# Optimization experiments

Measured on AMD Instinct MI355X. Metric: run time of the kernel, lower is better.

The kernel has to match this reference:

```python
import jax, jax.numpy as jnp
import numpy as np

EMB = 1024
HEADS = 16
HEAD_DIM = EMB // HEADS
SCALE = HEAD_DIM ** -0.5


def setup_inputs() -> dict:
    key = jax.random.key(0)
    ks = jax.random.split(key, 6)
    b, n = 4, 2048
    x = jax.random.normal(ks[0], (b, n, EMB), dtype=jnp.float32)
    ln_w = jnp.ones((EMB,), jnp.float32)
    ln_b = jnp.zeros((EMB,), jnp.float32)
    w_qkv = jax.random.normal(ks[1], (EMB, 3 * EMB), jnp.float32) * (EMB ** -0.5)
    b_qkv = jax.random.normal(ks[2], (3 * EMB,), jnp.float32) * 0.02
    w_proj = jax.random.normal(ks[3], (EMB, EMB), jnp.float32) * (EMB ** -0.5)
    b_proj = jax.random.normal(ks[4], (EMB,), jnp.float32) * 0.02
    return {"x": x, "ln_w": ln_w, "ln_b": ln_b, "w_qkv": w_qkv,
            "b_qkv": b_qkv, "w_proj": w_proj, "b_proj": b_proj}


def reference(x, ln_w, ln_b, w_qkv, b_qkv, w_proj, b_proj):
    res = x
    # LayerNorm over last dim
    mu = jnp.mean(x, axis=-1, keepdims=True)
    var = jnp.var(x, axis=-1, keepdims=True)
    h = (x - mu) * jax.lax.rsqrt(var + 1e-5) * ln_w + ln_b
    b, n, _ = h.shape
    # qkv: last dim split as (heads, head_dim, 3) -- qkv interleaved fastest
    y = h @ w_qkv + b_qkv                      # [b, n, 3E]
    y = y.reshape(b, n, HEADS, HEAD_DIM, 3)
    q, k, v = y[..., 0], y[..., 1], y[..., 2]  # [b, n, h, d]
    scores = jnp.einsum('bqhd,bkhd->bhqk', q, k) * SCALE
    att = jax.nn.softmax(scores, axis=-1)      # dropout p=0 -> identity
    out = jnp.einsum('bhqk,bkhd->bqhd', att, v)
    out = out.reshape(b, n, EMB)
    out = out @ w_proj + b_proj
    return out + res
```

## Files before the change

### kernel.cpp

```cpp
#include <hip/hip_runtime.h>
#include <math.h>

#define EMB 1024
#define HEADS 16
#define HDIM 64
#define NBATCH 4
#define SEQ 2048
#define ROWS (NBATCH * SEQ)
#define SCALE 0.125f
#define QPRESCALE 0.18033688011112042f

typedef float f32x4 __attribute__((ext_vector_type(4)));
typedef float f32x16 __attribute__((ext_vector_type(16)));
typedef short bf16x8 __attribute__((ext_vector_type(8)));

__device__ inline unsigned short f2bf(float f) {
    unsigned int u = __builtin_bit_cast(unsigned int, f);
    u += 0x7fffu + ((u >> 16) & 1u);
    return (unsigned short)(u >> 16);
}
__device__ inline float exp2fast(float x) {
    float y;
    asm("v_exp_f32 %0, %1" : "=v"(y) : "v"(x));
    return y;
}
__device__ inline unsigned int packbf(float x, float y) {
    return __builtin_amdgcn_perm(__builtin_bit_cast(unsigned int, y),
                                 __builtin_bit_cast(unsigned int, x), 0x07060302u);
}
__device__ inline bf16x8 mkfrag(unsigned int a, unsigned int b,
                                unsigned int c, unsigned int d) {
    union { unsigned int u[4]; bf16x8 v; } t;
    t.u[0] = a; t.u[1] = b; t.u[2] = c; t.u[3] = d;
    return t.v;
}

__global__ __launch_bounds__(256) void ln_kernel(const float* __restrict__ x,
                                                 const float* __restrict__ w,
                                                 const float* __restrict__ b,
                                                 unsigned short* __restrict__ h) {
    int row = blockIdx.x;
    const float* xr = x + (size_t)row * EMB;
    unsigned short* hr = h + (size_t)row * EMB;
    float4 v = ((const float4*)xr)[threadIdx.x];
    float s  = v.x + v.y + v.z + v.w;
    float ss = v.x*v.x + v.y*v.y + v.z*v.z + v.w*v.w;
    #pragma unroll
    for (int o = 32; o; o >>= 1) { s += __shfl_xor(s, o); ss += __shfl_xor(ss, o); }
    __shared__ float red[8];
    int wid = threadIdx.x >> 6;
    if ((threadIdx.x & 63) == 0) { red[wid] = s; red[4 + wid] = ss; }
    __syncthreads();
    if (threadIdx.x == 0) {
        red[0] = red[0] + red[1] + red[2] + red[3];
        red[4] = red[4] + red[5] + red[6] + red[7];
    }
    __syncthreads();
    float mu  = red[0] * (1.f / EMB);
    float var = red[4] * (1.f / EMB) - mu * mu;
    float rstd = rsqrtf(var + 1e-5f);
    float4 wv = ((const float4*)w)[threadIdx.x];
    float4 bv = ((const float4*)b)[threadIdx.x];
    ushort4 o;
    o.x = f2bf((v.x - mu) * rstd * wv.x + bv.x);
    o.y = f2bf((v.y - mu) * rstd * wv.y + bv.y);
    o.z = f2bf((v.z - mu) * rstd * wv.z + bv.z);
    o.w = f2bf((v.w - mu) * rstd * wv.w + bv.w);
    ((ushort4*)hr)[threadIdx.x] = o;
}

__global__ __launch_bounds__(256) void wconv(const float* __restrict__ W,
                                             unsigned short* __restrict__ WT,
                                             int N, int perm) {
    __shared__ float t[32][33];
    int k0 = blockIdx.x * 32, n0 = blockIdx.y * 32;
    int tx = threadIdx.x & 31, ty = threadIdx.x >> 5;
    #pragma unroll
    for (int i = 0; i < 32; i += 8)
        t[ty + i][tx] = W[(size_t)(k0 + ty + i) * N + n0 + tx];
    __syncthreads();
    #pragma unroll
    for (int i = 0; i < 32; i += 8) {
        int n = n0 + ty + i;
        int dst = n;
        if (perm) {
            int head = n / 192;
            int rem = n - head * 192;
            int d = rem / 3;
            int which = rem - d * 3;
            dst = which * 1024 + head * 64 + d;
        }
        WT[(size_t)dst * EMB + k0 + tx] = f2bf(t[tx][ty + i]);
    }
}

#define GSTAGE(LDSBUF, GPTR) do {                                                              \
    _Pragma("unroll")                                                                          \
    for (int i_ = 0; i_ < 2; ++i_) {                                                           \
        int slot_ = i_ * 256 + tid;                                                            \
        int row_ = slot_ >> 2, c8_ = (slot_ & 3) * 8;                                          \
        __builtin_amdgcn_global_load_lds(                                                      \
            (const __attribute__((address_space(1))) void*)((GPTR) + (size_t)row_ * EMB + c8_),\
            (__attribute__((address_space(3))) void*)((char*)(LDSBUF) + i_ * 4096 + w * 1024), \
            16, 0, 0);                                                                         \
    }                                                                                          \
} while (0)

__global__ __launch_bounds__(256) void qkv_mfma(const unsigned short* __restrict__ A,
                                                const unsigned short* __restrict__ BT,
                                                const float* __restrict__ bias,
                                                unsigned short* __restrict__ qo,
                                                unsigned short* __restrict__ ko,
                                                unsigned short* __restrict__ vo) {
    __shared__ alignas(16) unsigned short As[128][32];
    __shared__ alignas(16) unsigned short Bs[128][32];
    int tid = threadIdx.x;
    int w = tid >> 6, lane = tid & 63, lg = lane >> 4, lr = lane & 15;
    int wr = w >> 1, wc = w & 1;
    int bid = blockIdx.x;
    int local = bid >> 3;
    int bm = (bid & 7) * 8 + (local & 7);
    int bn = local >> 3;
    const unsigned short* Ab = A + (size_t)(bm * 128) * EMB;
    const unsigned short* Bb = BT + (size_t)(bn * 128) * EMB;
    f32x4 acc[4][4];
    #pragma unroll
    for (int m = 0; m < 4; ++m)
        #pragma unroll
        for (int n = 0; n < 4; ++n) acc[m][n] = (f32x4){0.f, 0.f, 0.f, 0.f};
    for (int k0 = 0; k0 < EMB; k0 += 32) {
        GSTAGE(As, Ab + k0);
        GSTAGE(Bs, Bb + k0);
        __syncthreads();
        bf16x8 af[4], bf[4];
        #pragma unroll
        for (int m = 0; m < 4; ++m) af[m] = *(const bf16x8*)&As[wr * 64 + m * 16 + lr][lg * 8];
        #pragma unroll
        for (int n = 0; n < 4; ++n) bf[n] = *(const bf16x8*)&Bs[wc * 64 + n * 16 + lr][lg * 8];
        #pragma unroll
        for (int m = 0; m < 4; ++m)
            #pragma unroll
            for (int n = 0; n < 4; ++n)
                acc[m][n] = __builtin_amdgcn_mfma_f32_16x16x32_bf16(af[m], bf[n], acc[m][n], 0, 0, 0);
        __syncthreads();
    }
    #pragma unroll
    for (int n = 0; n < 4; ++n) {
        int cp = bn * 128 + wc * 64 + n * 16 + lr;
        int which = cp >> 10;
        int head = (cp >> 6) & 15;
        int d = cp & 63;
        float bv = bias[head * 192 + d * 3 + which];
        #pragma unroll
        for (int m = 0; m < 4; ++m) {
            #pragma unroll
            for (int r = 0; r < 4; ++r) {
                int row = bm * 128 + wr * 64 + m * 16 + lg * 4 + r;
                int bb = row >> 11;
                int nq = row & 2047;
                float val = acc[m][n][r] + bv;
                if (which == 0)
                    qo[(((size_t)bb * HEADS + head) * SEQ + nq) * HDIM + d] = f2bf(val * QPRESCALE);
                else if (which == 1)
                    ko[(((size_t)bb * HEADS + head) * SEQ + nq) * HDIM + d] = f2bf(val);
                else
                    vo[(((size_t)bb * HEADS + head) * HDIM + d) * SEQ + nq] = f2bf(val);
            }
        }
    }
}

#define STAGE(nb, kb_) do {                                                                        \
    int off_ = sbase + lane * 16;                                   \
    int row_ = off_ >> 7;                                                                          \
    int lg_  = off_ ^ ((row_ & 7) << 4);                            \
    __builtin_amdgcn_global_load_lds(                                                              \
        (const __attribute__((address_space(1))) void*)(kbytes + (size_t)(kb_) * 8192 + lg_),      \
        (__attribute__((address_space(3))) void*)(&kls[nb][sbase]), 16, 0, 0);                     \
    __builtin_amdgcn_global_load_lds(                                                              \
        (const __attribute__((address_space(1))) void*)(vbytes + (size_t)row_ * (SEQ * 2)          \
                                         + (size_t)(kb_) * 128 + (lg_ & 127)),                     \
        (__attribute__((address_space(3))) void*)(&vls[nb][sbase]), 16, 0, 0);                     \
} while (0)

__global__ __launch_bounds__(512) void attn_mfma(const unsigned short* __restrict__ Q,
                                                 const unsigned short* __restrict__ K,
                                                 const unsigned short* __restrict__ VT,
                                                 unsigned short* __restrict__ AO) {
    __shared__ alignas(16) unsigned char kls[2][8192];
    __shared__ alignas(16) unsigned char vls[2][8192];
    int tid = threadIdx.x;
    int w = tid >> 6, lane = tid & 63;
    int col = lane & 31;
    int hi  = lane >> 5;
    int bid = blockIdx.x;
    int swz = (bid & 7) * 64 + (bid >> 3);
    int b  = swz >> 7;
    int hh = (swz >> 3) & 15;
    int qt = swz & 7;
    int q0 = qt * 256 + w * 32;
    size_t bh = ((size_t)b * HEADS + hh) * (size_t)SEQ * HDIM;
    const unsigned short* qp = Q + bh + (size_t)(q0 + col) * HDIM + 8 * hi;
    bf16x8 qB0 = *(const bf16x8*)(qp);
    bf16x8 qB1 = *(const bf16x8*)(qp + 16);
    bf16x8 qB2 = *(const bf16x8*)(qp + 32);
    bf16x8 qB3 = *(const bf16x8*)(qp + 48);
    f32x16 o0 = {0.f,0.f,0.f,0.f,0.f,0.f,0.f,0.f,0.f,0.f,0.f,0.f,0.f,0.f,0.f,0.f};
    f32x16 o1 = {0.f,0.f,0.f,0.f,0.f,0.f,0.f,0.f,0.f,0.f,0.f,0.f,0.f,0.f,0.f,0.f};
    float l = 0.f;
    const char* kbytes = (const char*)(K + bh);
    const char* vbytes = (const char*)(VT + bh);
    const int NT = SEQ / 64;
    int sbase = w * 1024;

    STAGE(0, 0);
    __syncthreads();
    for (int kb = 0; kb < NT; ++kb) {
        int cur = kb & 1;
        if (kb + 1 < NT) STAGE(cur ^ 1, kb + 1);
        const char* kcur = (const char*)&kls[cur][0];
        const char* vcur = (const char*)&vls[cur][0];
        #pragma unroll
        for (int t = 0; t < 2; ++t) {
            int keyl = t * 32 + col;
            int ksw = (keyl & 7) << 4;
            int kbs = keyl * 128;
            bf16x8 kf0 = *(const bf16x8*)(kcur + ((kbs +  0 + hi * 16) ^ ksw));
            bf16x8 kf1 = *(const bf16x8*)(kcur + ((kbs + 32 + hi * 16) ^ ksw));
            bf16x8 kf2 = *(const bf16x8*)(kcur + ((kbs + 64 + hi * 16) ^ ksw));
            bf16x8 kf3 = *(const bf16x8*)(kcur + ((kbs + 96 + hi * 16) ^ ksw));
            f32x16 s = {0.f,0.f,0.f,0.f,0.f,0.f,0.f,0.f,0.f,0.f,0.f,0.f,0.f,0.f,0.f,0.f};
            __builtin_amdgcn_s_setprio(1);
            s = __builtin_amdgcn_mfma_f32_32x32x16_bf16(kf0, qB0, s, 0, 0, 0);
            s = __builtin_amdgcn_mfma_f32_32x32x16_bf16(kf1, qB1, s, 0, 0, 0);
            s = __builtin_amdgcn_mfma_f32_32x32x16_bf16(kf2, qB2, s, 0, 0, 0);
            s = __builtin_amdgcn_mfma_f32_32x32x16_bf16(kf3, qB3, s, 0, 0, 0);
            __builtin_amdgcn_s_setprio(0);
            float p[16];
            float lsa = 0.f, lsb = 0.f;
            #pragma unroll
            for (int r = 0; r < 16; r += 2) {
                p[r]     = exp2fast(s[r]);
                p[r + 1] = exp2fast(s[r + 1]);
                lsa += p[r];
                lsb += p[r + 1];
            }
            l += lsa + lsb;
            unsigned int pk0 = packbf(p[0], p[1]),   pk1 = packbf(p[2], p[3]);
            unsigned int pk2 = packbf(p[4], p[5]),   pk3 = packbf(p[6], p[7]);
            unsigned int pk4 = packbf(p[8], p[9]),   pk5 = packbf(p[10], p[11]);
            unsigned int pk6 = packbf(p[12], p[13]), pk7 = packbf(p[14], p[15]);
            asm volatile("v_permlane32_swap_b32 %0, %1" : "+v"(pk0), "+v"(pk2));
            asm volatile("v_permlane32_swap_b32 %0, %1" : "+v"(pk1), "+v"(pk3));
            asm volatile("v_permlane32_swap_b32 %0, %1" : "+v"(pk4), "+v"(pk6));
            asm volatile("v_permlane32_swap_b32 %0, %1" : "+v"(pk5), "+v"(pk7));
            bf16x8 pf0 = mkfrag(pk0, pk1, pk2, pk3);
            bf16x8 pf1 = mkfrag(pk4, pk5, pk6, pk7);
            int vsw = (col & 7) << 4;
            int vb0 = col * 128 + t * 64;
            int vb1 = (32 + col) * 128 + t * 64;
            bf16x8 vf00 = *(const bf16x8*)(vcur + ((vb0 + hi * 16) ^ vsw));
            bf16x8 vf01 = *(const bf16x8*)(vcur + ((vb0 + 32 + hi * 16) ^ vsw));
            bf16x8 vf10 = *(const bf16x8*)(vcur + ((vb1 + hi * 16) ^ vsw));
            bf16x8 vf11 = *(const bf16x8*)(vcur + ((vb1 + 32 + hi * 16) ^ vsw));
            __builtin_amdgcn_s_setprio(1);
            o0 = __builtin_amdgcn_mfma_f32_32x32x16_bf16(pf0, vf00, o0, 0, 0, 0);
            o0 = __builtin_amdgcn_mfma_f32_32x32x16_bf16(pf1, vf01, o0, 0, 0, 0);
            o1 = __builtin_amdgcn_mfma_f32_32x32x16_bf16(pf0, vf10, o1, 0, 0, 0);
            o1 = __builtin_amdgcn_mfma_f32_32x32x16_bf16(pf1, vf11, o1, 0, 0, 0);
            __builtin_amdgcn_s_setprio(0);
        }
        if (kb + 1 < NT) __syncthreads();
    }
    float invc = 1.f / (l + __shfl_xor(l, 32));
    #pragma unroll
    for (int reg = 0; reg < 16; ++reg) {
        int crow = (reg & 3) + 8 * (reg >> 2) + 4 * hi;
        float invr = __shfl(invc, crow);
        int qq = q0 + crow;
        unsigned short* op = AO + ((size_t)b * SEQ + qq) * EMB + hh * HDIM + col;
        op[0]  = f2bf(o0[reg] * invr);
        op[32] = f2bf(o1[reg] * invr);
    }
}

__global__ __launch_bounds__(256) void proj_mfma(const unsigned short* __restrict__ A,
                                                 const unsigned short* __restrict__ BT,
                                                 const float* __restrict__ bias,
                                                 const float* __restrict__ resid,
                                                 float* __restrict__ out) {
    __shared__ alignas(16) unsigned short As[128][32];
    __shared__ alignas(16) unsigned short Bs[128][32];
    int tid = threadIdx.x;
    int w = tid >> 6, lane = tid & 63, lg = lane >> 4, lr = lane & 15;
    int wr = w >> 1, wc = w & 1;
    int bid = blockIdx.x;
    int local = bid >> 3;
    int bm = (bid & 7) * 8 + (local & 7);
    int bn = local >> 3;
    const unsigned short* Ab = A + (size_t)(bm * 128) * EMB;
    const unsigned short* Bb = BT + (size_t)(bn * 128) * EMB;
    f32x4 acc[4][4];
    #pragma unroll
    for (int m = 0; m < 4; ++m)
        #pragma unroll
        for (int n = 0; n < 4; ++n) acc[m][n] = (f32x4){0.f, 0.f, 0.f, 0.f};
    for (int k0 = 0; k0 < EMB; k0 += 32) {
        GSTAGE(As, Ab + k0);
        GSTAGE(Bs, Bb + k0);
        __syncthreads();
        bf16x8 af[4], bf[4];
        #pragma unroll
        for (int m = 0; m < 4; ++m) af[m] = *(const bf16x8*)&As[wr * 64 + m * 16 + lr][lg * 8];
        #pragma unroll
        for (int n = 0; n < 4; ++n) bf[n] = *(const bf16x8*)&Bs[wc * 64 + n * 16 + lr][lg * 8];
        #pragma unroll
        for (int m = 0; m < 4; ++m)
            #pragma unroll
            for (int n = 0; n < 4; ++n)
                acc[m][n] = __builtin_amdgcn_mfma_f32_16x16x32_bf16(af[m], bf[n], acc[m][n], 0, 0, 0);
        __syncthreads();
    }
    #pragma unroll
    for (int n = 0; n < 4; ++n) {
        int c = bn * 128 + wc * 64 + n * 16 + lr;
        float bv = bias[c];
        #pragma unroll
        for (int m = 0; m < 4; ++m) {
            #pragma unroll
            for (int r = 0; r < 4; ++r) {
                size_t row = (size_t)bm * 128 + wr * 64 + m * 16 + lg * 4 + r;
                out[row * EMB + c] = acc[m][n][r] + bv + resid[row * EMB + c];
            }
        }
    }
}

extern "C" void kernel_launch(void* const* d_in, const int* in_sizes, int n_in,
                              void* d_out, int out_size, void* d_ws, size_t ws_size,
                              hipStream_t stream) {
    const float* x      = (const float*)d_in[0];
    const float* ln_w   = (const float*)d_in[1];
    const float* ln_b   = (const float*)d_in[2];
    const float* w_qkv  = (const float*)d_in[3];
    const float* b_qkv  = (const float*)d_in[4];
    const float* w_proj = (const float*)d_in[5];
    const float* b_proj = (const float*)d_in[6];
    float* out = (float*)d_out;

    char* ws = (char*)d_ws;
    const size_t MB16 = (size_t)ROWS * EMB * sizeof(unsigned short);
    unsigned short* h   = (unsigned short*)ws;
    unsigned short* q   = (unsigned short*)(ws + MB16);
    unsigned short* k   = (unsigned short*)(ws + 2 * MB16);
    unsigned short* v   = (unsigned short*)(ws + 3 * MB16);
    unsigned short* ao  = (unsigned short*)(ws + 4 * MB16);
    unsigned short* wqT = (unsigned short*)(ws + 5 * MB16);
    unsigned short* wpT = (unsigned short*)(ws + 5 * MB16 + (size_t)3 * EMB * EMB * 2);

    wconv<<<dim3(EMB / 32, 3 * EMB / 32), 256, 0, stream>>>(w_qkv, wqT, 3 * EMB, 1);
    wconv<<<dim3(EMB / 32, EMB / 32), 256, 0, stream>>>(w_proj, wpT, EMB, 0);
    ln_kernel<<<ROWS, 256, 0, stream>>>(x, ln_w, ln_b, h);
    qkv_mfma<<<1536, 256, 0, stream>>>(h, wqT, b_qkv, q, k, v);
    attn_mfma<<<512, 512, 0, stream>>>(q, k, v, ao);
    proj_mfma<<<512, 256, 0, stream>>>(ao, wpT, b_proj, x, out);
}
```

Baseline: 219.8 us.

## Double-buffer LDS tiles in QKV and projection GEMMs to overlap loads with MFMA

Both GEMM kernels now use two LDS buffers per operand and issue the global-to-LDS loads for the next K tile before computing on the current one. This drops one barrier per iteration and is meant to hide global load latency behind MFMA work. The cost is doubled LDS use per block, which can lower occupancy. There is also a risk of ordering hazards, because the async global_load_lds writes are only ordered by the single remaining barrier.

After: 230.9 us. 1.05x slower.

```diff
diff --git a/kernel.cpp b/kernel.cpp
--- a/kernel.cpp
+++ b/kernel.cpp
@@ -112,8 +112,8 @@
                                                 unsigned short* __restrict__ qo,
                                                 unsigned short* __restrict__ ko,
                                                 unsigned short* __restrict__ vo) {
-    __shared__ alignas(16) unsigned short As[128][32];
-    __shared__ alignas(16) unsigned short Bs[128][32];
+    __shared__ alignas(16) unsigned short As[2][128][32];
+    __shared__ alignas(16) unsigned short Bs[2][128][32];
     int tid = threadIdx.x;
     int w = tid >> 6, lane = tid & 63, lg = lane >> 4, lr = lane & 15;
     int wr = w >> 1, wc = w & 1;
@@ -128,21 +128,27 @@
     for (int m = 0; m < 4; ++m)
         #pragma unroll
         for (int n = 0; n < 4; ++n) acc[m][n] = (f32x4){0.f, 0.f, 0.f, 0.f};
-    for (int k0 = 0; k0 < EMB; k0 += 32) {
-        GSTAGE(As, Ab + k0);
-        GSTAGE(Bs, Bb + k0);
-        __syncthreads();
+    const int NI = EMB / 32;
+    GSTAGE(As[0], Ab);
+    GSTAGE(Bs[0], Bb);
+    __syncthreads();
+    for (int it = 0; it < NI; ++it) {
+        int cur = it & 1;
+        if (it + 1 < NI) {
+            GSTAGE(As[cur ^ 1], Ab + (it + 1) * 32);
+            GSTAGE(Bs[cur ^ 1], Bb + (it + 1) * 32);
+        }
         bf16x8 af[4], bf[4];
         #pragma unroll
-        for (int m = 0; m < 4; ++m) af[m] = *(const bf16x8*)&As[wr * 64 + m * 16 + lr][lg * 8];
-        #pragma unroll
-        for (int n = 0; n < 4; ++n) bf[n] = *(const bf16x8*)&Bs[wc * 64 + n * 16 + lr][lg * 8];
+        for (int m = 0; m < 4; ++m) af[m] = *(const bf16x8*)&As[cur][wr * 64 + m * 16 + lr][lg * 8];
+        #pragma unroll
+        for (int n = 0; n < 4; ++n) bf[n] = *(const bf16x8*)&Bs[cur][wc * 64 + n * 16 + lr][lg * 8];
         #pragma unroll
         for (int m = 0; m < 4; ++m)
             #pragma unroll
             for (int n = 0; n < 4; ++n)
                 acc[m][n] = __builtin_amdgcn_mfma_f32_16x16x32_bf16(af[m], bf[n], acc[m][n], 0, 0, 0);
-        __syncthreads();
+        if (it + 1 < NI) __syncthreads();
     }
     #pragma unroll
     for (int n = 0; n < 4; ++n) {
@@ -289,8 +295,8 @@
                                                  const float* __restrict__ bias,
                                                  const float* __restrict__ resid,
                                                  float* __restrict__ out) {
-    __shared__ alignas(16) unsigned short As[128][32];
-    __shared__ alignas(16) unsigned short Bs[128][32];
+    __shared__ alignas(16) unsigned short As[2][128][32];
+    __shared__ alignas(16) unsigned short Bs[2][128][32];
     int tid = threadIdx.x;
     int w = tid >> 6, lane = tid & 63, lg = lane >> 4, lr = lane & 15;
     int wr = w >> 1, wc = w & 1;
@@ -305,21 +311,27 @@
     for (int m = 0; m < 4; ++m)
         #pragma unroll
         for (int n = 0; n < 4; ++n) acc[m][n] = (f32x4){0.f, 0.f, 0.f, 0.f};
-    for (int k0 = 0; k0 < EMB; k0 += 32) {
-        GSTAGE(As, Ab + k0);
-        GSTAGE(Bs, Bb + k0);
-        __syncthreads();
+    const int NI = EMB / 32;
+    GSTAGE(As[0], Ab);
+    GSTAGE(Bs[0], Bb);
+    __syncthreads();
+    for (int it = 0; it < NI; ++it) {
+        int cur = it & 1;
+        if (it + 1 < NI) {
+            GSTAGE(As[cur ^ 1], Ab + (it + 1) * 32);
+            GSTAGE(Bs[cur ^ 1], Bb + (it + 1) * 32);
+        }
         bf16x8 af[4], bf[4];
         #pragma unroll
-        for (int m = 0; m < 4; ++m) af[m] = *(const bf16x8*)&As[wr * 64 + m * 16 + lr][lg * 8];
-        #pragma unroll
-        for (int n = 0; n < 4; ++n) bf[n] = *(const bf16x8*)&Bs[wc * 64 + n * 16 + lr][lg * 8];
+        for (int m = 0; m < 4; ++m) af[m] = *(const bf16x8*)&As[cur][wr * 64 + m * 16 + lr][lg * 8];
+        #pragma unroll
+        for (int n = 0; n < 4; ++n) bf[n] = *(const bf16x8*)&Bs[cur][wc * 64 + n * 16 + lr][lg * 8];
         #pragma unroll
         for (int m = 0; m < 4; ++m)
             #pragma unroll
             for (int n = 0; n < 4; ++n)
                 acc[m][n] = __builtin_amdgcn_mfma_f32_16x16x32_bf16(af[m], bf[n], acc[m][n], 0, 0, 0);
-        __syncthreads();
+        if (it + 1 < NI) __syncthreads();
     }
     #pragma unroll
     for (int n = 0; n < 4; ++n) {
```

## Double K-tile depth to 64 and XOR-swizzle LDS layout in GEMM kernels

Applied to the files above, without the earlier changes.

The QKV and projection GEMMs now stage a 64-wide K slice per iteration instead of 32. This halves the number of barrier pairs and the loop overhead, and each sync is followed by two MFMA sub-steps. The LDS tile is laid out with an XOR swizzle on the 16-byte column chunk, keyed by row, so the 128-byte row stride does not cause bank conflicts on fragment reads. LDS use per block doubles to 32 KB, which could reduce occupancy.

New measurement: 214.9 us. 2.2% less time.

```diff
diff --git a/kernel.cpp b/kernel.cpp
--- a/kernel.cpp
+++ b/kernel.cpp
@@ -94,13 +94,15 @@
     }
 }
 
-#define GSTAGE(LDSBUF, GPTR) do {                                                              \
+#define GSTAGE64(LDSBUF, GPTR) do {                                                            \
     _Pragma("unroll")                                                                          \
-    for (int i_ = 0; i_ < 2; ++i_) {                                                           \
-        int slot_ = i_ * 256 + tid;                                                            \
-        int row_ = slot_ >> 2, c8_ = (slot_ & 3) * 8;                                          \
+    for (int i_ = 0; i_ < 4; ++i_) {                                                           \
+        int phys_ = (i_ * 256 + tid) * 16;                              \
+        int row_ = phys_ >> 7;                                                     \
+        int lg_  = (phys_ & 127) ^ ((row_ & 7) << 4);                                          \
         __builtin_amdgcn_global_load_lds(                                                      \
-            (const __attribute__((address_space(1))) void*)((GPTR) + (size_t)row_ * EMB + c8_),\
+            (const __attribute__((address_space(1))) void*)                                    \
+                ((const char*)(GPTR) + (size_t)row_ * (EMB * 2) + lg_),                        \
             (__attribute__((address_space(3))) void*)((char*)(LDSBUF) + i_ * 4096 + w * 1024), \
             16, 0, 0);                                                                         \
     }                                                                                          \
@@ -112,8 +114,8 @@
                                                 unsigned short* __restrict__ qo,
                                                 unsigned short* __restrict__ ko,
                                                 unsigned short* __restrict__ vo) {
-    __shared__ alignas(16) unsigned short As[128][32];
-    __shared__ alignas(16) unsigned short Bs[128][32];
+    __shared__ alignas(16) unsigned char As[16384];
+    __shared__ alignas(16) unsigned char Bs[16384];
     int tid = threadIdx.x;
     int w = tid >> 6, lane = tid & 63, lg = lane >> 4, lr = lane & 15;
     int wr = w >> 1, wc = w & 1;
@@ -128,20 +130,31 @@
     for (int m = 0; m < 4; ++m)
         #pragma unroll
         for (int n = 0; n < 4; ++n) acc[m][n] = (f32x4){0.f, 0.f, 0.f, 0.f};
-    for (int k0 = 0; k0 < EMB; k0 += 32) {
-        GSTAGE(As, Ab + k0);
-        GSTAGE(Bs, Bb + k0);
+    for (int k0 = 0; k0 < EMB; k0 += 64) {
+        GSTAGE64(As, Ab + k0);
+        GSTAGE64(Bs, Bb + k0);
         __syncthreads();
-        bf16x8 af[4], bf[4];
-        #pragma unroll
-        for (int m = 0; m < 4; ++m) af[m] = *(const bf16x8*)&As[wr * 64 + m * 16 + lr][lg * 8];
-        #pragma unroll
-        for (int n = 0; n < 4; ++n) bf[n] = *(const bf16x8*)&Bs[wc * 64 + n * 16 + lr][lg * 8];
-        #pragma unroll
-        for (int m = 0; m < 4; ++m)
-            #pragma unroll
-            for (int n = 0; n < 4; ++n)
-                acc[m][n] = __builtin_amdgcn_mfma_f32_16x16x32_bf16(af[m], bf[n], acc[m][n], 0, 0, 0);
+        #pragma unroll
+        for (int kk = 0; kk < 2; ++kk) {
+            bf16x8 af[4], bf[4];
+            #pragma unroll
+            for (int m = 0; m < 4; ++m) {
+                int arow = wr * 64 + m * 16 + lr;
+                int ab = arow * 128 + ((lg * 16 + kk * 64) ^ ((arow & 7) << 4));
+                af[m] = *(const bf16x8*)(As + ab);
+            }
+            #pragma unroll
+            for (int n = 0; n < 4; ++n) {
+                int brow = wc * 64 + n * 16 + lr;
+                int bb2 = brow * 128 + ((lg * 16 + kk * 64) ^ ((brow & 7) << 4));
+                bf[n] = *(const bf16x8*)(Bs + bb2);
+            }
+            #pragma unroll
+            for (int m = 0; m < 4; ++m)
+                #pragma unroll
+                for (int n = 0; n < 4; ++n)
+                    acc[m][n] = __builtin_amdgcn_mfma_f32_16x16x32_bf16(af[m], bf[n], acc[m][n], 0, 0, 0);
+        }
         __syncthreads();
     }
     #pragma unroll
@@ -289,8 +302,8 @@
                                                  const float* __restrict__ bias,
                                                  const float* __restrict__ resid,
                                                  float* __restrict__ out) {
-    __shared__ alignas(16) unsigned short As[128][32];
-    __shared__ alignas(16) unsigned short Bs[128][32];
+    __shared__ alignas(16) unsigned char As[16384];
+    __shared__ alignas(16) unsigned char Bs[16384];
     int tid = threadIdx.x;
     int w = tid >> 6, lane = tid & 63, lg = lane >> 4, lr = lane & 15;
     int wr = w >> 1, wc = w & 1;
@@ -305,20 +318,31 @@
     for (int m = 0; m < 4; ++m)
         #pragma unroll
         for (int n = 0; n < 4; ++n) acc[m][n] = (f32x4){0.f, 0.f, 0.f, 0.f};
-    for (int k0 = 0; k0 < EMB; k0 += 32) {
-        GSTAGE(As, Ab + k0);
-        GSTAGE(Bs, Bb + k0);
+    for (int k0 = 0; k0 < EMB; k0 += 64) {
+        GSTAGE64(As, Ab + k0);
+        GSTAGE64(Bs, Bb + k0);
         __syncthreads();
-        bf16x8 af[4], bf[4];
-        #pragma unroll
-        for (int m = 0; m < 4; ++m) af[m] = *(const bf16x8*)&As[wr * 64 + m * 16 + lr][lg * 8];
-        #pragma unroll
-        for (int n = 0; n < 4; ++n) bf[n] = *(const bf16x8*)&Bs[wc * 64 + n * 16 + lr][lg * 8];
-        #pragma unroll
-        for (int m = 0; m < 4; ++m)
-            #pragma unroll
-            for (int n = 0; n < 4; ++n)
-                acc[m][n] = __builtin_amdgcn_mfma_f32_16x16x32_bf16(af[m], bf[n], acc[m][n], 0, 0, 0);
+        #pragma unroll
+        for (int kk = 0; kk < 2; ++kk) {
+            bf16x8 af[4], bf[4];
+            #pragma unroll
+            for (int m = 0; m < 4; ++m) {
+                int arow = wr * 64 + m * 16 + lr;
+                int ab = arow * 128 + ((lg * 16 + kk * 64) ^ ((arow & 7) << 4));
+                af[m] = *(const bf16x8*)(As + ab);
+            }
+            #pragma unroll
+            for (int n = 0; n < 4; ++n) {
+                int brow = wc * 64 + n * 16 + lr;
+                int bb2 = brow * 128 + ((lg * 16 + kk * 64) ^ ((brow & 7) << 4));
+                bf[n] = *(const bf16x8*)(Bs + bb2);
+            }
+            #pragma unroll
+            for (int m = 0; m < 4; ++m)
+                #pragma unroll
+                for (int n = 0; n < 4; ++n)
+                    acc[m][n] = __builtin_amdgcn_mfma_f32_16x16x32_bf16(af[m], bf[n], acc[m][n], 0, 0, 0);
+        }
         __syncthreads();
     }
     #pragma unroll
```
